# Kernel optimization log

Measured on AMD Instinct MI355X. Metric: run time of the kernel, lower is better.

The kernel has to match this reference:

```python
import jax, jax.numpy as jnp
import numpy as np

SEQ, B, D, T = 512, 128, 1024, 32  # seq_len, batch, input_dim, num_tags


def setup_inputs() -> dict:
    key = jax.random.key(0)
    ks = jax.random.split(key, 6)
    return {
        "features": jax.random.normal(ks[0], (SEQ, B, D), jnp.float32),
        "mask": jnp.ones((SEQ, B), jnp.int32),
        "W": jax.random.normal(ks[1], (T, D), jnp.float32) * 0.02,   # features_to_tag weight
        "b": jnp.zeros((T,), jnp.float32),                            # features_to_tag bias
        "transition": jax.random.normal(ks[2], (T, T), jnp.float32) * 0.1,
        "start_probs": jax.random.normal(ks[3], (T,), jnp.float32) * 0.1,
        "end_probs": jax.random.normal(ks[4], (T,), jnp.float32) * 0.1,
    }


def _alpha(emissions, maskf, trans, start):
    # forward recursion: alpha[i, b, j] = logsumexp_k(alpha[i-1,b,k] + trans[k,j]) + e[i,b,j]
    a0 = emissions[0] + start[None, :]
    def step(prev, xs):
        e, m = xs
        new = jax.nn.logsumexp(prev[:, :, None] + trans[None] + e[:, None, :], axis=1)
        nxt = m[:, None] * new + (1.0 - m)[:, None] * prev
        return nxt, nxt
    _, rest = jax.lax.scan(step, a0, (emissions[1:], maskf[1:]))
    return jnp.concatenate([a0[None], rest], axis=0)  # (S,B,T)


def _beta(emissions, maskf, trans, end):
    # backward recursion: beta[i-1, b, j] = logsumexp_k(beta[i,b,k] + e[i,b,k] + trans[j,k])
    bL = jnp.broadcast_to(end[None, :], emissions.shape[1:])  # (B,T)
    def step(prev, xs):
        e, m = xs
        s = prev + e  # (B,T)
        new = jax.nn.logsumexp(s[:, None, :] + trans[None], axis=2)
        nxt = m[:, None] * new + (1.0 - m)[:, None] * prev
        return nxt, nxt
    _, rest = jax.lax.scan(step, bL, (emissions[1:], maskf[1:]), reverse=True)
    return jnp.concatenate([rest, bL[None]], axis=0)  # (S,B,T)


def _viterbi(emissions, mask, trans, start, end):
    s0 = start[None, :] + emissions[0]  # (B,T)
    def step(score, xs):
        e, m = xs
        cand = score[:, :, None] + trans[None] + e[:, None, :]  # (B,T_from,T_to)
        nxt = jnp.max(cand, axis=1)
        idx = jnp.argmax(cand, axis=1).astype(jnp.int32)
        score = jnp.where(m[:, None].astype(bool), nxt, score)
        return score, idx
    score, history = jax.lax.scan(step, s0, (emissions[1:], mask[1:]))
    score = score + end[None, :]
    last = jnp.argmax(score, axis=1).astype(jnp.int32)  # (B,)
    def back(tag, hist):
        new = jnp.take_along_axis(hist, tag[:, None], axis=1)[:, 0]
        return new, new
    _, tags_rest = jax.lax.scan(back, last, history, reverse=True)
    return jnp.concatenate([tags_rest, last[None]], axis=0)  # (S,B)


def reference(features, mask, W, b, transition, start_probs, end_probs):
    emissions = jnp.einsum("sbd,td->sbt", features, W) + b  # (S,B,T)
    maskf = mask.astype(emissions.dtype)
    alpha = _alpha(emissions, maskf, transition, start_probs)
    beta = _beta(emissions, maskf, transition, end_probs)
    z = jax.nn.logsumexp(alpha[-1] + end_probs[None, :], axis=1)  # (B,)
    probs = jnp.exp(alpha + beta - z[None, :, None])  # marginal probabilities
    tags = _viterbi(emissions, mask, transition, start_probs, end_probs)
    return probs, tags
```

## Files before the change

### kernel.cpp

```cpp
#include <hip/hip_runtime.h>

#define SEQ 512
#define BATCH 128
#define DIM 1024
#define T 32

__device__ __forceinline__ float rlf(float x, int n) {
    return __int_as_float(__builtin_amdgcn_readlane(__float_as_int(x), n));
}

__device__ __forceinline__ int mbit(unsigned long long m0, unsigned long long m1,
        unsigned long long m2, unsigned long long m3, unsigned long long m4,
        unsigned long long m5, unsigned long long m6, unsigned long long m7, int i) {
    int w = i >> 6;
    unsigned long long cm =
        (w < 4) ? ((w < 2) ? (w == 0 ? m0 : m1) : (w == 2 ? m2 : m3))
                : ((w < 6) ? (w == 4 ? m4 : m5) : (w == 6 ? m6 : m7));
    return (int)((cm >> (i & 63)) & 1ULL);
}

#define BALLOTS(pre, bb) \
    unsigned long long pre##0 = __ballot(mask[(0 * 64 + tid) * BATCH + (bb)] != 0); \
    unsigned long long pre##1 = __ballot(mask[(1 * 64 + tid) * BATCH + (bb)] != 0); \
    unsigned long long pre##2 = __ballot(mask[(2 * 64 + tid) * BATCH + (bb)] != 0); \
    unsigned long long pre##3 = __ballot(mask[(3 * 64 + tid) * BATCH + (bb)] != 0); \
    unsigned long long pre##4 = __ballot(mask[(4 * 64 + tid) * BATCH + (bb)] != 0); \
    unsigned long long pre##5 = __ballot(mask[(5 * 64 + tid) * BATCH + (bb)] != 0); \
    unsigned long long pre##6 = __ballot(mask[(6 * 64 + tid) * BATCH + (bb)] != 0); \
    unsigned long long pre##7 = __ballot(mask[(7 * 64 + tid) * BATCH + (bb)] != 0);

#define MB(pre, i) mbit(pre##0, pre##1, pre##2, pre##3, pre##4, pre##5, pre##6, pre##7, (i))

#define MATVEC32(dst, src, Et) { \
    float q0 = 0.f, q1 = 0.f, q2 = 0.f, q3 = 0.f; \
    _Pragma("unroll") \
    for (int n = 0; n < 8; ++n) { \
        q0 = fmaf(rlf(src, 4 * n + 0), Et[4 * n + 0], q0); \
        q1 = fmaf(rlf(src, 4 * n + 1), Et[4 * n + 1], q1); \
        q2 = fmaf(rlf(src, 4 * n + 2), Et[4 * n + 2], q2); \
        q3 = fmaf(rlf(src, 4 * n + 3), Et[4 * n + 3], q3); \
    } \
    dst = (q0 + q1) + (q2 + q3); }

#define RLSUM32(dst, src) { \
    float s0 = 0.f, s1 = 0.f, s2 = 0.f, s3 = 0.f; \
    _Pragma("unroll") \
    for (int n = 0; n < 8; ++n) { \
        s0 += rlf(src, 4 * n + 0); \
        s1 += rlf(src, 4 * n + 1); \
        s2 += rlf(src, 4 * n + 2); \
        s3 += rlf(src, 4 * n + 3); \
    } \
    dst = (s0 + s1) + (s2 + s3); }

#define STAGEXP(blk) do { \
    _Pragma("unroll") \
    for (int ps = 0; ps < 16; ++ps) { \
        int r = ps * 8 + r8; \
        float4 v = *(const float4*)&e[(size_t)(((blk) * 128 + r) * BATCH + b) * T + q * 4]; \
        v.x = __expf(v.x); v.y = __expf(v.y); v.z = __expf(v.z); v.w = __expf(v.w); \
        *(float4*)&ebuf[(blk) & 1][r * 32 + q * 4] = v; \
    } } while (0)

#define FLUSHPC(dstP, dstC, blk) do { \
    _Pragma("unroll") \
    for (int ps = 0; ps < 16; ++ps) { \
        int r = ps * 8 + r8; \
        float4 v = *(const float4*)&pbuf[(blk) & 1][r * 32 + q * 4]; \
        *(float4*)&dstP[(size_t)(((blk) * 128 + r) * BATCH + b) * T + q * 4] = v; \
    } \
    _Pragma("unroll") \
    for (int ps = 0; ps < 2; ++ps) { \
        int r = ps * 64 + tid; \
        dstC[(size_t)((blk) * 128 + r) * BATCH + b] = cbuf[(blk) & 1][r]; \
    } } while (0)

#define STAGEV(blk) do { \
    _Pragma("unroll") \
    for (int ps = 0; ps < 8; ++ps) { \
        int r = ps * 8 + r8; \
        float4 v = *(const float4*)&e[(size_t)(((blk) * 64 + r) * BATCH + b2) * T + q * 4]; \
        *(float4*)&ebufv[r * 32 + q * 4] = v; \
    } } while (0)

__global__ void k_wt(const float* __restrict__ W, float* __restrict__ Wt)
{
    int idx = blockIdx.x * 256 + threadIdx.x;
    if (idx >= DIM * T) return;
    int d = idx >> 5, t = idx & 31;
    Wt[idx] = W[t * DIM + d];
}

__global__ __launch_bounds__(256) void k_emis(const float* __restrict__ A,
        const float* __restrict__ Wt, const float* __restrict__ bias,
        float* __restrict__ e)
{
    __shared__ float lds[64 * 37];
    int tid = threadIdx.x;
    int row0 = blockIdx.x * 64;
    int row = tid & 63;
    int grp = __builtin_amdgcn_readfirstlane(tid >> 6);
    int q = tid & 7;
    int rb = tid >> 3;

    float acc[8];
    #pragma unroll
    for (int t = 0; t < 8; ++t) acc[t] = bias[grp * 8 + t];

    const float* A0 = &A[(size_t)(row0 + rb) * DIM];
    const float* A1 = &A[(size_t)(row0 + rb + 32) * DIM];

    float4 v0 = *(const float4*)&A0[q * 4];
    float4 v1 = *(const float4*)&A1[q * 4];

    for (int ck = 0; ck < 32; ++ck) {
        lds[rb * 37 + q * 4 + 0] = v0.x;
        lds[rb * 37 + q * 4 + 1] = v0.y;
        lds[rb * 37 + q * 4 + 2] = v0.z;
        lds[rb * 37 + q * 4 + 3] = v0.w;
        lds[(rb + 32) * 37 + q * 4 + 0] = v1.x;
        lds[(rb + 32) * 37 + q * 4 + 1] = v1.y;
        lds[(rb + 32) * 37 + q * 4 + 2] = v1.z;
        lds[(rb + 32) * 37 + q * 4 + 3] = v1.w;
        __syncthreads();
        if (ck < 31) {
            v0 = *(const float4*)&A0[(ck + 1) * 32 + q * 4];
            v1 = *(const float4*)&A1[(ck + 1) * 32 + q * 4];
        }
        #pragma unroll
        for (int d = 0; d < 32; ++d) {
            float av = lds[row * 37 + d];
            const float* wrow = &Wt[(ck * 32 + d) * T + grp * 8];
            #pragma unroll
            for (int t = 0; t < 8; ++t)
                acc[t] = fmaf(av, wrow[t], acc[t]);
        }
        __syncthreads();
    }

    float4* eo = (float4*)&e[(size_t)(row0 + row) * T + grp * 8];
    float4 o0, o1;
    o0.x = acc[0]; o0.y = acc[1]; o0.z = acc[2]; o0.w = acc[3];
    o1.x = acc[4]; o1.y = acc[5]; o1.z = acc[6]; o1.w = acc[7];
    eo[0] = o0; eo[1] = o1;
}

__global__ __launch_bounds__(64) void k_rec(const float* __restrict__ e,
        const int* __restrict__ mask,
        const float* __restrict__ trans,
        const float* __restrict__ start,
        const float* __restrict__ endp,
        float* __restrict__ pa, float* __restrict__ pb,
        double* __restrict__ Ca, double* __restrict__ Cb,
        double* __restrict__ zd,
        float* __restrict__ tags_out)
{
    __shared__ __align__(16) char smem[78336];
    int bid = blockIdx.x;
    int tid = threadIdx.x;
    int j   = tid & 31;
    int r8 = tid >> 3, q = tid & 7;

    if (bid < 256) {
        int role = bid >> 7;
        int b    = bid & 127;
        float (*ebuf)[4096] = (float(*)[4096])smem;
        float (*pbuf)[4096] = (float(*)[4096])(smem + 32768);
        double (*cbuf)[128] = (double(*)[128])(smem + 65536);

        BALLOTS(ma, b);
        float Et[32];

        if (role == 0) {
            #pragma unroll
            for (int n = 0; n < 32; ++n) Et[n] = __expf(trans[n * T + j]);

            STAGEXP(0);
            float a0 = e[(0 * BATCH + b) * T + j] + start[j];
            float m = a0;
            #pragma unroll
            for (int d = 1; d < 32; d <<= 1) m = fmaxf(m, __shfl_xor(m, d));
            float v = __expf(a0 - m);
            float s = v;
            #pragma unroll
            for (int d = 1; d < 32; d <<= 1) s += __shfl_xor(s, d);
            float p = v / s;
            double C = (double)m + (double)__logf(s);
            if (tid < 32) pbuf[0][j] = p;
            if (tid == 0) cbuf[0][0] = C;

            for (int c = 0; c < 4; ++c) {
                int i0 = c ? c * 128 : 1, i1 = c * 128 + 127;
                for (int i = i0; i <= i1; ++i) {
                    float ee = ebuf[c & 1][(i & 127) * 32 + j];
                    float q_;
                    MATVEC32(q_, p, Et);
                    float vv = q_ * ee;
                    if (MB(ma, i)) p = vv;
                    if (tid < 32) pbuf[c & 1][(i & 127) * 32 + j] = p;
                    if (tid == 0) cbuf[c & 1][i & 127] = C;
                    if ((i & 7) == 0) {
                        float ss; RLSUM32(ss, p);
                        p = p / ss; C += (double)__logf(ss);
                    }
                }
                if (c < 3) STAGEXP(c + 1);
                FLUSHPC(pa, Ca, c);
            }
            float sz0 = p * __expf(endp[j]);
            float sz; RLSUM32(sz, sz0);
            if (tid == 0) zd[b] = C + (double)__logf(sz);
        } else {
            #pragma unroll
            for (int n = 0; n < 32; ++n) Et[n] = __expf(trans[j * T + n]);

            STAGEXP(3);
            float v0 = endp[j];
            float m = v0;
            #pragma unroll
            for (int d = 1; d < 32; d <<= 1) m = fmaxf(m, __shfl_xor(m, d));
            float v = __expf(v0 - m);
            float s = v;
            #pragma unroll
            for (int d = 1; d < 32; d <<= 1) s += __shfl_xor(s, d);
            float p = v / s;
            double C = (double)m + (double)__logf(s);
            if (tid < 32) pbuf[1][127 * 32 + j] = p;
            if (tid == 0) cbuf[1][127] = C;

            float een = ebuf[1][127 * 32 + j];
            for (int c = 0; c < 4; ++c) {
                int iS = 511 - 128 * c;
                int iE = (c < 3) ? (384 - 128 * c) : 1;
                for (int i = iS; i >= iE; --i) {
                    float ee = een;
                    if (i > iE)
                        een = ebuf[((i - 1) >> 7) & 1][((i - 1) & 127) * 32 + j];
                    float pe = p * ee;
                    float q_;
                    MATVEC32(q_, pe, Et);
                    if (MB(ma, i)) p = q_;
                    int orow = i - 1, lb = (orow >> 7) & 1;
                    if (tid < 32) pbuf[lb][(orow & 127) * 32 + j] = p;
                    if (tid == 0) cbuf[lb][orow & 127] = C;
                    if ((i & 7) == 0) {
                        float ss; RLSUM32(ss, p);
                        p = p / ss; C += (double)__logf(ss);
                    }
                }
                if (c < 3) {
                    STAGEXP(2 - c);
                    een = ebuf[(2 - c) & 1][127 * 32 + j];
                }
                FLUSHPC(pb, Cb, 3 - c);
            }
        }
    } else {
        int b2 = bid - 256;
        float* ebufv = (float*)smem;
        float* sbuf  = (float*)(smem + 8192);
        float* tldsT = (float*)(smem + 73728);
        unsigned char* tagb = (unsigned char*)(smem + 77824);

        BALLOTS(ma, b2);

        #pragma unroll
        for (int k = 0; k < 16; ++k) {
            int idx = k * 64 + tid;
            int nn = idx >> 5, jj = idx & 31;
            tldsT[jj * 32 + nn] = trans[nn * T + jj];
        }

        float trv[32];
        #pragma unroll
        for (int n = 0; n < 32; ++n) trv[n] = trans[n * T + j];

        STAGEV(0);
        float sc = start[j] + ebufv[j];
        if (tid < 32) sbuf[j] = sc;

        for (int c = 0; c < 8; ++c) {
            int i0 = c ? c * 64 : 1, i1 = c * 64 + 63;
            for (int i = i0; i <= i1; ++i) {
                const float4* srow = (const float4*)&sbuf[(i - 1) * 32];
                float ej = ebufv[(i & 63) * 32 + j];
                float cc[32];
                #pragma unroll
                for (int w4 = 0; w4 < 8; ++w4) {
                    float4 sv = srow[w4];
                    cc[4 * w4 + 0] = sv.x + trv[4 * w4 + 0];
                    cc[4 * w4 + 1] = sv.y + trv[4 * w4 + 1];
                    cc[4 * w4 + 2] = sv.z + trv[4 * w4 + 2];
                    cc[4 * w4 + 3] = sv.w + trv[4 * w4 + 3];
                }
                float t[11];
                #pragma unroll
                for (int g = 0; g < 10; ++g)
                    t[g] = fmaxf(fmaxf(cc[3 * g], cc[3 * g + 1]), cc[3 * g + 2]);
                t[10] = fmaxf(cc[30], cc[31]);
                float u0 = fmaxf(fmaxf(t[0], t[1]), t[2]);
                float u1 = fmaxf(fmaxf(t[3], t[4]), t[5]);
                float u2 = fmaxf(fmaxf(t[6], t[7]), t[8]);
                float u3 = fmaxf(t[9], t[10]);
                float m_ = fmaxf(fmaxf(u0, u1), fmaxf(u2, u3));
                float v = m_ + ej;
                if (MB(ma, i)) sc = v;
                if (tid < 32) sbuf[i * 32 + j] = sc;
            }
            if (c < 7) STAGEV(c + 1);
        }

        float fs = sc + endp[j];
        int fj = j;
        #pragma unroll
        for (int d = 1; d < 32; d <<= 1) {
            float ov = __shfl_xor(fs, d); int oj = __shfl_xor(fj, d);
            if (ov > fs || (ov == fs && oj < fj)) { fs = ov; fj = oj; }
        }
        int jstar = __builtin_amdgcn_readfirstlane(fj);
        tagb[SEQ - 1] = (unsigned char)jstar;

        int n = tid & 31;
        for (int c = 7; c >= 0; --c) {
            if (c < 7) STAGEV(c);
            int iS = c * 64 + 63, iE = c ? c * 64 : 1;
            for (int i = iS; i >= iE; --i) {
                float sn = sbuf[(i - 1) * 32 + n];
                float tn = tldsT[jstar * 32 + n];
                float en = ebufv[(i & 63) * 32 + jstar];
                float cn = (sn + tn) + en;
                float v;
                if (MB(ma, i)) {
                    v = sbuf[i * 32 + jstar];
                } else {
                    v = cn;
                    #pragma unroll
                    for (int d = 1; d < 32; d <<= 1)
                        v = fmaxf(v, __shfl_xor(v, d));
                }
                unsigned long long bm = __ballot(cn == v);
                jstar = (int)__builtin_ctzll(bm);
                tagb[i - 1] = (unsigned char)jstar;
            }
        }
        #pragma unroll
        for (int k2 = 0; k2 < 8; ++k2) {
            int idx = k2 * 64 + tid;
            tags_out[(size_t)idx * BATCH + b2] = (float)tagb[idx];
        }
    }
}

__global__ __launch_bounds__(256) void k_probs(const float* __restrict__ pa,
        const float* __restrict__ pb, const double* __restrict__ Ca,
        const double* __restrict__ Cb, const double* __restrict__ zd,
        float* __restrict__ out)
{
    int idx = blockIdx.x * 256 + threadIdx.x;
    int ib = idx >> 3;
    int b = ib & (BATCH - 1);
    double ex = Ca[ib] + Cb[ib] - zd[b];
    double scl = exp(ex);
    float4 a = ((const float4*)pa)[idx];
    float4 c = ((const float4*)pb)[idx];
    float4 o;
    o.x = (float)((double)a.x * (double)c.x * scl);
    o.y = (float)((double)a.y * (double)c.y * scl);
    o.z = (float)((double)a.z * (double)c.z * scl);
    o.w = (float)((double)a.w * (double)c.w * scl);
    ((float4*)out)[idx] = o;
}

extern "C" void kernel_launch(void* const* d_in, const int* in_sizes, int n_in,
                              void* d_out, int out_size, void* d_ws, size_t ws_size,
                              hipStream_t stream) {
    const float* features = (const float*)d_in[0];
    const int*   mask     = (const int*)d_in[1];
    const float* W        = (const float*)d_in[2];
    const float* bias     = (const float*)d_in[3];
    const float* trans    = (const float*)d_in[4];
    const float* startp   = (const float*)d_in[5];
    const float* endp     = (const float*)d_in[6];

    char* ws = (char*)d_ws;
    double* Ca = (double*)(ws + 0);
    double* Cb = (double*)(ws + 524288);
    double* zd = (double*)(ws + 1048576);
    float*  Wt = (float*)(ws + 1049600);
    float*  e  = (float*)(ws + 1180672);
    float*  pa = (float*)(ws + 9569280);
    float*  pb = (float*)(ws + 17957888);

    float* probs_out = (float*)d_out;
    float* tags_out  = probs_out + (size_t)SEQ * BATCH * T;

    k_wt<<<128, 256, 0, stream>>>(W, Wt);
    k_emis<<<1024, 256, 0, stream>>>(features, Wt, bias, e);
    k_rec<<<384, 64, 0, stream>>>(e, mask, trans, startp, endp,
                                  pa, pb, Ca, Cb, zd, tags_out);
    k_probs<<<2048, 256, 0, stream>>>(pa, pb, Ca, Cb, zd, probs_out);
}
```

Before: 314.3 us.

## Split per-step 32-term reductions across both wave halves via LDS reads

The forward, backward and Viterbi recursions previously had each lane do a full 32-term matvec or max over the previous state, broadcast through readlane. Now the two 32-lane halves of the wave each handle 16 of the source tags, read the previous state as float4s from the LDS buffer, and combine the halves with a cross-half shuffle. This halves the per-step dependent chain and removes the readlane broadcasts. The cost is a write-then-read through LDS on every step, which puts LDS latency on the serial critical path, and the pbuf/cbuf stores are moved after the renormalisation so the stored state is the normalised one.

```diff
diff --git a/kernel.cpp b/kernel.cpp
--- a/kernel.cpp
+++ b/kernel.cpp
@@ -30,17 +30,6 @@
     unsigned long long pre##7 = __ballot(mask[(7 * 64 + tid) * BATCH + (bb)] != 0);
 
 #define MB(pre, i) mbit(pre##0, pre##1, pre##2, pre##3, pre##4, pre##5, pre##6, pre##7, (i))
-
-#define MATVEC32(dst, src, Et) { \
-    float q0 = 0.f, q1 = 0.f, q2 = 0.f, q3 = 0.f; \
-    _Pragma("unroll") \
-    for (int n = 0; n < 8; ++n) { \
-        q0 = fmaf(rlf(src, 4 * n + 0), Et[4 * n + 0], q0); \
-        q1 = fmaf(rlf(src, 4 * n + 1), Et[4 * n + 1], q1); \
-        q2 = fmaf(rlf(src, 4 * n + 2), Et[4 * n + 2], q2); \
-        q3 = fmaf(rlf(src, 4 * n + 3), Et[4 * n + 3], q3); \
-    } \
-    dst = (q0 + q1) + (q2 + q3); }
 
 #define RLSUM32(dst, src) { \
     float s0 = 0.f, s1 = 0.f, s2 = 0.f, s3 = 0.f; \
@@ -159,6 +148,7 @@
     int bid = blockIdx.x;
     int tid = threadIdx.x;
     int j   = tid & 31;
+    int h   = tid >> 5;
     int r8 = tid >> 3, q = tid & 7;
 
     if (bid < 256) {
@@ -169,11 +159,12 @@
         double (*cbuf)[128] = (double(*)[128])(smem + 65536);
 
         BALLOTS(ma, b);
-        float Et[32];
+        float Eh[16];
 
         if (role == 0) {
             #pragma unroll
-            for (int n = 0; n < 32; ++n) Et[n] = __expf(trans[n * T + j]);
+            for (int m = 0; m < 16; ++m)
+                Eh[m] = __expf(trans[(16 * h + m) * T + j]);
 
             STAGEXP(0);
             float a0 = e[(0 * BATCH + b) * T + j] + start[j];
@@ -192,17 +183,24 @@
             for (int c = 0; c < 4; ++c) {
                 int i0 = c ? c * 128 : 1, i1 = c * 128 + 127;
                 for (int i = i0; i <= i1; ++i) {
+                    int pr = i - 1;
+                    const float4* pr4 = (const float4*)&pbuf[(pr >> 7) & 1][(pr & 127) * 32 + 16 * h];
                     float ee = ebuf[c & 1][(i & 127) * 32 + j];
-                    float q_;
-                    MATVEC32(q_, p, Et);
-                    float vv = q_ * ee;
+                    float4 x0 = pr4[0], x1 = pr4[1], x2 = pr4[2], x3 = pr4[3];
+                    float q0 = fmaf(x0.w, Eh[3], fmaf(x0.z, Eh[2], fmaf(x0.y, Eh[1], x0.x * Eh[0])));
+                    float q1 = fmaf(x1.w, Eh[7], fmaf(x1.z, Eh[6], fmaf(x1.y, Eh[5], x1.x * Eh[4])));
+                    float q2 = fmaf(x2.w, Eh[11], fmaf(x2.z, Eh[10], fmaf(x2.y, Eh[9], x2.x * Eh[8])));
+                    float q3 = fmaf(x3.w, Eh[15], fmaf(x3.z, Eh[14], fmaf(x3.y, Eh[13], x3.x * Eh[12])));
+                    float qh = (q0 + q1) + (q2 + q3);
+                    float qq = qh + __shfl_xor(qh, 32);
+                    float vv = qq * ee;
                     if (MB(ma, i)) p = vv;
-                    if (tid < 32) pbuf[c & 1][(i & 127) * 32 + j] = p;
-                    if (tid == 0) cbuf[c & 1][i & 127] = C;
                     if ((i & 7) == 0) {
                         float ss; RLSUM32(ss, p);
                         p = p / ss; C += (double)__logf(ss);
                     }
+                    if (tid < 32) pbuf[c & 1][(i & 127) * 32 + j] = p;
+                    if (tid == 0) cbuf[c & 1][i & 127] = C;
                 }
                 if (c < 3) STAGEXP(c + 1);
                 FLUSHPC(pa, Ca, c);
@@ -212,7 +210,8 @@
             if (tid == 0) zd[b] = C + (double)__logf(sz);
         } else {
             #pragma unroll
-            for (int n = 0; n < 32; ++n) Et[n] = __expf(trans[j * T + n]);
+            for (int m = 0; m < 16; ++m)
+                Eh[m] = __expf(trans[j * T + 16 * h + m]);
 
             STAGEXP(3);
             float v0 = endp[j];
@@ -228,30 +227,35 @@
             if (tid < 32) pbuf[1][127 * 32 + j] = p;
             if (tid == 0) cbuf[1][127] = C;
 
-            float een = ebuf[1][127 * 32 + j];
             for (int c = 0; c < 4; ++c) {
                 int iS = 511 - 128 * c;
                 int iE = (c < 3) ? (384 - 128 * c) : 1;
                 for (int i = iS; i >= iE; --i) {
-                    float ee = een;
-                    if (i > iE)
-                        een = ebuf[((i - 1) >> 7) & 1][((i - 1) & 127) * 32 + j];
-                    float pe = p * ee;
-                    float q_;
-                    MATVEC32(q_, pe, Et);
-                    if (MB(ma, i)) p = q_;
-                    int orow = i - 1, lb = (orow >> 7) & 1;
-                    if (tid < 32) pbuf[lb][(orow & 127) * 32 + j] = p;
-                    if (tid == 0) cbuf[lb][orow & 127] = C;
+                    int bI = (i >> 7) & 1;
+                    const float4* pr4 = (const float4*)&pbuf[bI][(i & 127) * 32 + 16 * h];
+                    const float4* er4 = (const float4*)&ebuf[bI][(i & 127) * 32 + 16 * h];
+                    float4 pv0 = pr4[0], pv1 = pr4[1], pv2 = pr4[2], pv3 = pr4[3];
+                    float4 ev0 = er4[0], ev1 = er4[1], ev2 = er4[2], ev3 = er4[3];
+                    float q0 = fmaf(pv0.w * ev0.w, Eh[3], fmaf(pv0.z * ev0.z, Eh[2],
+                                fmaf(pv0.y * ev0.y, Eh[1], (pv0.x * ev0.x) * Eh[0])));
+                    float q1 = fmaf(pv1.w * ev1.w, Eh[7], fmaf(pv1.z * ev1.z, Eh[6],
+                                fmaf(pv1.y * ev1.y, Eh[5], (pv1.x * ev1.x) * Eh[4])));
+                    float q2 = fmaf(pv2.w * ev2.w, Eh[11], fmaf(pv2.z * ev2.z, Eh[10],
+                                fmaf(pv2.y * ev2.y, Eh[9], (pv2.x * ev2.x) * Eh[8])));
+                    float q3 = fmaf(pv3.w * ev3.w, Eh[15], fmaf(pv3.z * ev3.z, Eh[14],
+                                fmaf(pv3.y * ev3.y, Eh[13], (pv3.x * ev3.x) * Eh[12])));
+                    float qh = (q0 + q1) + (q2 + q3);
+                    float qq = qh + __shfl_xor(qh, 32);
+                    if (MB(ma, i)) p = qq;
                     if ((i & 7) == 0) {
                         float ss; RLSUM32(ss, p);
                         p = p / ss; C += (double)__logf(ss);
                     }
+                    int orow = i - 1, lb = (orow >> 7) & 1;
+                    if (tid < 32) pbuf[lb][(orow & 127) * 32 + j] = p;
+                    if (tid == 0) cbuf[lb][orow & 127] = C;
                 }
-                if (c < 3) {
-                    STAGEXP(2 - c);
-                    een = ebuf[(2 - c) & 1][127 * 32 + j];
-                }
+                if (c < 3) STAGEXP(2 - c);
                 FLUSHPC(pb, Cb, 3 - c);
             }
         }
@@ -271,9 +275,10 @@
             tldsT[jj * 32 + nn] = trans[nn * T + jj];
         }
 
-        float trv[32];
-        #pragma unroll
-        for (int n = 0; n < 32; ++n) trv[n] = trans[n * T + j];
+        float trvh[16];
+        #pragma unroll
+        for (int m = 0; m < 16; ++m)
+            trvh[m] = trans[(16 * h + m) * T + j];
 
         STAGEV(0);
         float sc = start[j] + ebufv[j];
@@ -282,28 +287,20 @@
         for (int c = 0; c < 8; ++c) {
             int i0 = c ? c * 64 : 1, i1 = c * 64 + 63;
             for (int i = i0; i <= i1; ++i) {
-                const float4* srow = (const float4*)&sbuf[(i - 1) * 32];
+                const float4* sr4 = (const float4*)&sbuf[(i - 1) * 32 + 16 * h];
                 float ej = ebufv[(i & 63) * 32 + j];
-                float cc[32];
-                #pragma unroll
-                for (int w4 = 0; w4 < 8; ++w4) {
-                    float4 sv = srow[w4];
-                    cc[4 * w4 + 0] = sv.x + trv[4 * w4 + 0];
-                    cc[4 * w4 + 1] = sv.y + trv[4 * w4 + 1];
-                    cc[4 * w4 + 2] = sv.z + trv[4 * w4 + 2];
-                    cc[4 * w4 + 3] = sv.w + trv[4 * w4 + 3];
-                }
-                float t[11];
-                #pragma unroll
-                for (int g = 0; g < 10; ++g)
-                    t[g] = fmaxf(fmaxf(cc[3 * g], cc[3 * g + 1]), cc[3 * g + 2]);
-                t[10] = fmaxf(cc[30], cc[31]);
-                float u0 = fmaxf(fmaxf(t[0], t[1]), t[2]);
-                float u1 = fmaxf(fmaxf(t[3], t[4]), t[5]);
-                float u2 = fmaxf(fmaxf(t[6], t[7]), t[8]);
-                float u3 = fmaxf(t[9], t[10]);
-                float m_ = fmaxf(fmaxf(u0, u1), fmaxf(u2, u3));
-                float v = m_ + ej;
+                float4 s0 = sr4[0], s1 = sr4[1], s2 = sr4[2], s3 = sr4[3];
+                float m0 = fmaxf(fmaxf(s0.x + trvh[0], s0.y + trvh[1]),
+                                 fmaxf(s0.z + trvh[2], s0.w + trvh[3]));
+                float m1 = fmaxf(fmaxf(s1.x + trvh[4], s1.y + trvh[5]),
+                                 fmaxf(s1.z + trvh[6], s1.w + trvh[7]));
+                float m2 = fmaxf(fmaxf(s2.x + trvh[8], s2.y + trvh[9]),
+                                 fmaxf(s2.z + trvh[10], s2.w + trvh[11]));
+                float m3 = fmaxf(fmaxf(s3.x + trvh[12], s3.y + trvh[13]),
+                                 fmaxf(s3.z + trvh[14], s3.w + trvh[15]));
+                float mh = fmaxf(fmaxf(m0, m1), fmaxf(m2, m3));
+                float mm = fmaxf(mh, __shfl_xor(mh, 32));
+                float v = mm + ej;
                 if (MB(ma, i)) sc = v;
                 if (tid < 32) sbuf[i * 32 + j] = sc;
             }
```

Result: faster. 288.8 us (-8.1%).
